# Optimization experiments

Measured on AMD Instinct MI355X. Metric: run time of the kernel, lower is better.

## Reference

```python
import jax, jax.numpy as jnp
import numpy as np

N_ING, N_DIR = 100000, 50000
E = 1000000
H, D = 4, 16          # heads, per-head dim
HID = H * D           # 64
LAT, COND = 32, 8
F_ING, F_DIR = 16, 8
OUT_ING = 16


def _han_edge(x_src, x_dst, att_s, att_d, edge_index, n_dst):
    # HANConv per-edge-type attention message passing.
    src, dst = edge_index[0], edge_index[1]
    a = jax.nn.leaky_relu(
        jnp.einsum('nhd,hd->nh', x_src, att_s)[src]
        + jnp.einsum('nhd,hd->nh', x_dst, att_d)[dst],
        negative_slope=0.2)                               # [E, H]
    amax = jax.ops.segment_max(a, dst, num_segments=n_dst)
    ex = jnp.exp(a - amax[dst])
    denom = jax.ops.segment_sum(ex, dst, num_segments=n_dst)
    alpha = ex / (denom[dst] + 1e-16)                     # PyG softmax eps
    out = jax.ops.segment_sum(x_src[src] * alpha[:, :, None], dst,
                              num_segments=n_dst)         # [n_dst, H, D]
    return jax.nn.relu(out.reshape(n_dst, HID))


def _group(outs, q, Wk, bk):
    # HANConv semantic-level attention across edge types.
    s = jnp.stack(outs)                                   # [T, N, HID]
    score = jnp.tanh(s @ Wk + bk).mean(axis=1) @ q        # [T]
    attn = jax.nn.softmax(score)
    return jnp.einsum('t,tnf->nf', attn, s)


def setup_inputs() -> dict:
    key = jax.random.key(0)
    ks = jax.random.split(key, 32)
    def ei(k, n_src, n_dst):
        k1, k2 = jax.random.split(k)
        return jnp.stack([jax.random.randint(k1, (E,), 0, n_src),
                          jax.random.randint(k2, (E,), 0, n_dst)]).astype(jnp.int64)
    s = 0.1
    inp = {
        'x_ing': jax.random.normal(ks[0], (N_ING, F_ING), jnp.float32),
        'x_dir': jax.random.normal(ks[1], (N_DIR, F_DIR), jnp.float32),
        'cond':  jax.random.normal(ks[2], (COND,), jnp.float32),
        'eps':   jax.random.normal(ks[3], (1, LAT), jnp.float32),
        'ei_cooc':     ei(ks[4], N_ING, N_DIR),
        'ei_used':     ei(ks[5], N_ING, N_DIR),
        'ei_contains': ei(ks[6], N_DIR, N_ING),
        'ei_pairs':    ei(ks[7], N_DIR, N_DIR),
        'ei_follows':  ei(ks[8], N_DIR, N_DIR),
        # node-type projections
        'W_pi': jax.random.normal(ks[9],  (F_ING, HID)) * s,
        'b_pi': jnp.zeros((HID,)),
        'W_pd': jax.random.normal(ks[10], (F_DIR, HID)) * s,
        'b_pd': jnp.zeros((HID,)),
        # semantic attention
        'Wk': jax.random.normal(ks[21], (HID, HID)) * s,
        'bk': jnp.zeros((HID,)),
        'q':  jax.random.normal(ks[22], (HID,)) * s,
        # VAE heads (input: 2*HID + COND)
        'W_mu': jax.random.normal(ks[23], (2 * HID + COND, LAT)) * s,
        'b_mu': jnp.zeros((LAT,)),
        'W_lv': jax.random.normal(ks[24], (2 * HID + COND, LAT)) * s,
        'b_lv': jnp.zeros((LAT,)),
        # decoder (fc1 is dead code in the original forward)
        'W_fc3': jax.random.normal(ks[25], (LAT, HID)) * s,
        'b_fc3': jnp.zeros((HID,)),
        'W_fc2': jax.random.normal(ks[26], (HID, OUT_ING)) * s,
        'b_fc2': jnp.zeros((OUT_ING,)),
    }
    for i, name in enumerate(['cooc', 'used', 'contains', 'pairs', 'follows']):
        inp[f'as_{name}'] = jax.random.normal(ks[11 + i], (H, D)) * s
        inp[f'ad_{name}'] = jax.random.normal(ks[16 + i], (H, D)) * s
    return inp


def reference(x_ing, x_dir, cond, eps,
              ei_cooc, ei_used, ei_contains, ei_pairs, ei_follows,
              W_pi, b_pi, W_pd, b_pd,
              as_cooc, ad_cooc, as_used, ad_used, as_contains, ad_contains,
              as_pairs, ad_pairs, as_follows, ad_follows,
              Wk, bk, q, W_mu, b_mu, W_lv, b_lv,
              W_fc3, b_fc3, W_fc2, b_fc2):
    # node-type projections -> [N, H, D]
    h_ing = (x_ing @ W_pi + b_pi).reshape(N_ING, H, D)
    h_dir = (x_dir @ W_pd + b_pd).reshape(N_DIR, H, D)

    o_cooc = _han_edge(h_ing, h_dir, as_cooc, ad_cooc, ei_cooc, N_DIR)
    o_used = _han_edge(h_ing, h_dir, as_used, ad_used, ei_used, N_DIR)
    o_cont = _han_edge(h_dir, h_ing, as_contains, ad_contains, ei_contains, N_ING)
    o_pair = _han_edge(h_dir, h_dir, as_pairs, ad_pairs, ei_pairs, N_DIR)
    o_foll = _han_edge(h_dir, h_dir, as_follows, ad_follows, ei_follows, N_DIR)

    out_ing = _group([o_cont], q, Wk, bk)                       # [N_ING, HID]
    out_dir = _group([o_cooc, o_used, o_pair, o_foll], q, Wk, bk)

    ingre_pool = out_ing.mean(axis=0, keepdims=True)            # [1, HID]
    direc_pool = out_dir.mean(axis=0, keepdims=True)
    graph_repr = jnp.concatenate([ingre_pool, direc_pool, cond[None]], axis=1)

    mu = graph_repr @ W_mu + b_mu
    logvar = graph_repr @ W_lv + b_lv
    z = mu + eps * jnp.exp(0.5 * logvar)

    # decoder: fc1 branch is overwritten in the original; effective path below
    recon = jnp.tanh(jax.nn.relu(z @ W_fc3 + b_fc3) @ W_fc2 + b_fc2)  # [1, OUT_ING]
    return recon, mu, logvar
```

## Files before the change

kernel.cpp:

```cpp
#include <hip/hip_runtime.h>
#include <hip/hip_fp16.h>
#include <math.h>

#define N_ING 100000
#define N_DIR 50000
#define NE    1000000
#define NDST_TOTAL 300000
#define NBUCK 4688
#define BA    32
#define NBK   (5 * BA)
#define I4PT  (NE / 4)
#define PB_ING 384
#define PB_DIR 192

typedef float v2f __attribute__((ext_vector_type(2)));

__global__ __launch_bounds__(256) void kA_kernel(
    const int* __restrict__ e0, const int* __restrict__ e1,
    const int* __restrict__ e2, const int* __restrict__ e3,
    const int* __restrict__ e4, int* __restrict__ blockcnt,
    const float* __restrict__ x_ing, const float* __restrict__ W_pi,
    const float* __restrict__ b_pi,
    const float* __restrict__ as_cooc, const float* __restrict__ as_used,
    const float* __restrict__ ad_contains,
    unsigned* __restrict__ h8_ing, __half* __restrict__ s_ing,
    const float* __restrict__ x_dir, const float* __restrict__ W_pd,
    const float* __restrict__ b_pd,
    const float* __restrict__ ad_cooc, const float* __restrict__ ad_used,
    const float* __restrict__ as_contains, const float* __restrict__ as_pairs,
    const float* __restrict__ ad_pairs, const float* __restrict__ as_follows,
    const float* __restrict__ ad_follows,
    unsigned* __restrict__ h8_dir, __half* __restrict__ s_dir)
{
    __shared__ int hist[NBUCK];
    __shared__ float sW[16 * 64];
    __shared__ float sbb[64];
    __shared__ float satt[7 * 64];
    __shared__ float sx[4][16];
    __shared__ float srow[4][64];

    const int bid = blockIdx.x;
    const int tid = threadIdx.x;
    if (bid < NBK) {
        const int type = bid / BA, blk = bid % BA;
        const int* ei = type == 0 ? e0 : type == 1 ? e1 : type == 2 ? e2
                      : type == 3 ? e3 : e4;
        const int base = type == 0 ? 0 : type == 1 ? 50000 : type == 2 ? 100000
                       : type == 3 ? 200000 : 250000;
        for (int i = tid; i < NBUCK; i += 256) hist[i] = 0;
        __syncthreads();
        const int4* d4 = (const int4*)(ei + NE);
        for (int i = blk * 256 + tid; i < I4PT; i += BA * 256) {
            int4 d = d4[i];
            atomicAdd(&hist[(base + d.x) >> 6], 1);
            atomicAdd(&hist[(base + d.y) >> 6], 1);
            atomicAdd(&hist[(base + d.z) >> 6], 1);
            atomicAdd(&hist[(base + d.w) >> 6], 1);
        }
        __syncthreads();
        int* row = blockcnt + (size_t)bid * NBUCK;
        for (int i = tid; i < NBUCK; i += 256) row[i] = hist[i];
    } else if (bid < NBK + PB_ING) {
        const int g = tid >> 6, t = tid & 63;
        for (int i = tid; i < 16 * 64; i += 256) sW[i] = W_pi[i];
        if (tid < 64) {
            sbb[tid] = b_pi[tid];
            satt[tid]       = as_cooc[tid];
            satt[64 + tid]  = as_used[tid];
            satt[128 + tid] = ad_contains[tid];
        }
        __syncthreads();
        for (int q = bid - NBK; q < N_ING / 4; q += PB_ING) {
            int n = q * 4 + g;
            if (t < 16) sx[g][t] = x_ing[(size_t)n * 16 + t];
            __syncthreads();
            float s = sbb[t];
#pragma unroll
            for (int i = 0; i < 16; ++i) s += sx[g][i] * sW[i * 64 + t];
            srow[g][t] = s;
            __syncthreads();
            if (t < 16) {
                int w0 = __builtin_amdgcn_cvt_pk_fp8_f32(srow[g][t * 4], srow[g][t * 4 + 1], 0, false);
                int w  = __builtin_amdgcn_cvt_pk_fp8_f32(srow[g][t * 4 + 2], srow[g][t * 4 + 3], w0, true);
                h8_ing[(size_t)n * 16 + t] = (unsigned)w;
            }
            if (t < 12) {
                int slot = t >> 2, hh = t & 3;
                float sc = 0.f;
#pragma unroll
                for (int d = 0; d < 16; ++d)
                    sc += srow[g][hh * 16 + d] * satt[slot * 64 + hh * 16 + d];
                s_ing[(size_t)n * 12 + t] = __float2half(sc);
            }
            __syncthreads();
        }
    } else {
        const int g = tid >> 6, t = tid & 63;
        for (int i = tid; i < 8 * 64; i += 256) sW[i] = W_pd[i];
        if (tid < 64) {
            sbb[tid] = b_pd[tid];
            satt[tid]        = ad_cooc[tid];
            satt[64  + tid]  = ad_used[tid];
            satt[128 + tid]  = as_contains[tid];
            satt[192 + tid]  = as_pairs[tid];
            satt[256 + tid]  = ad_pairs[tid];
            satt[320 + tid]  = as_follows[tid];
            satt[384 + tid]  = ad_follows[tid];
        }
        __syncthreads();
        for (int q = bid - NBK - PB_ING; q < N_DIR / 4; q += PB_DIR) {
            int n = q * 4 + g;
            if (t < 8) sx[g][t] = x_dir[(size_t)n * 8 + t];
            __syncthreads();
            float s = sbb[t];
#pragma unroll
            for (int i = 0; i < 8; ++i) s += sx[g][i] * sW[i * 64 + t];
            srow[g][t] = s;
            __syncthreads();
            if (t < 16) {
                int w0 = __builtin_amdgcn_cvt_pk_fp8_f32(srow[g][t * 4], srow[g][t * 4 + 1], 0, false);
                int w  = __builtin_amdgcn_cvt_pk_fp8_f32(srow[g][t * 4 + 2], srow[g][t * 4 + 3], w0, true);
                h8_dir[(size_t)n * 16 + t] = (unsigned)w;
            }
            if (t < 28) {
                int slot = t >> 2, hh = t & 3;
                float sc = 0.f;
#pragma unroll
                for (int d = 0; d < 16; ++d)
                    sc += srow[g][hh * 16 + d] * satt[slot * 64 + hh * 16 + d];
                s_dir[(size_t)n * 28 + t] = __float2half(sc);
            }
            __syncthreads();
        }
    }
}

__global__ __launch_bounds__(256) void k2_kernel(
    const int* __restrict__ blockcnt, int* __restrict__ blockbase,
    int* __restrict__ bbase, int* __restrict__ btot, int* __restrict__ cursor)
{
    __shared__ int part[4][64];
    __shared__ int tots[64];
    __shared__ int scn[64];
    __shared__ int bw;
    const int tid = threadIdx.x;
    const int kq = tid >> 6, bl = tid & 63;
    const int b = blockIdx.x * 64 + bl;
    const int K = NBK / 4;
    int ps = 0;
    if (b < NBUCK)
        for (int k = kq * K; k < kq * K + K; ++k)
            ps += blockcnt[(size_t)k * NBUCK + b];
    part[kq][bl] = ps;
    __syncthreads();
    if (tid < 64) {
        int t = part[0][tid] + part[1][tid] + part[2][tid] + part[3][tid];
        tots[tid] = t;
        scn[tid] = t;
    }
    __syncthreads();
    for (int off = 1; off < 64; off <<= 1) {
        int v = 0;
        if (tid < 64 && tid >= off) v = scn[tid - off];
        __syncthreads();
        if (tid < 64) scn[tid] += v;
        __syncthreads();
    }
    if (tid == 63) bw = atomicAdd(cursor, scn[63]);
    __syncthreads();
    if (b < NBUCK) {
        int bs = bw + scn[bl] - tots[bl];
        if (kq == 0) {
            bbase[b] = bs;
            btot[b] = tots[bl];
        }
        int run = bs;
        for (int q = 0; q < kq; ++q) run += part[q][bl];
        for (int k = kq * K; k < kq * K + K; ++k) {
            blockbase[(size_t)k * NBUCK + b] = run;
            run += blockcnt[(size_t)k * NBUCK + b];
        }
    }
}

__global__ __launch_bounds__(256) void k3_kernel(
    const int* __restrict__ e0, const int* __restrict__ e1,
    const int* __restrict__ e2, const int* __restrict__ e3,
    const int* __restrict__ e4, const int* __restrict__ blockbase,
    unsigned* __restrict__ bpair)
{
    __shared__ int cur[NBUCK];
    const int bid = blockIdx.x, tid = threadIdx.x;
    const int type = bid / BA, blk = bid % BA;
    const int* ei = type == 0 ? e0 : type == 1 ? e1 : type == 2 ? e2
                  : type == 3 ? e3 : e4;
    const int base = type == 0 ? 0 : type == 1 ? 50000 : type == 2 ? 100000
                   : type == 3 ? 200000 : 250000;
    const int* row = blockbase + (size_t)bid * NBUCK;
    for (int i = tid; i < NBUCK; i += 256) cur[i] = row[i];
    __syncthreads();
    const int4* s4 = (const int4*)ei;
    const int4* d4 = (const int4*)(ei + NE);
    for (int i = blk * 256 + tid; i < I4PT; i += BA * 256) {
        int4 s = s4[i];
        int4 d = d4[i];
        int g0 = base + d.x, g1 = base + d.y, g2 = base + d.z, g3 = base + d.w;
        int p0 = atomicAdd(&cur[g0 >> 6], 1);
        int p1 = atomicAdd(&cur[g1 >> 6], 1);
        int p2 = atomicAdd(&cur[g2 >> 6], 1);
        int p3 = atomicAdd(&cur[g3 >> 6], 1);
        bpair[p0] = ((unsigned)(g0 & 63) << 17) | (unsigned)s.x;
        bpair[p1] = ((unsigned)(g1 & 63) << 17) | (unsigned)s.y;
        bpair[p2] = ((unsigned)(g2 & 63) << 17) | (unsigned)s.z;
        bpair[p3] = ((unsigned)(g3 & 63) << 17) | (unsigned)s.w;
    }
}

__global__ __launch_bounds__(256) void k4_kernel(
    const unsigned* __restrict__ bpair, const int* __restrict__ bbase,
    const int* __restrict__ btot, int* __restrict__ perm,
    int* __restrict__ start, int* __restrict__ cnt)
{
    __shared__ int hw[4][64];
    __shared__ int sc[64];
    __shared__ int cuw[4][64];
    const int b = blockIdx.x, tid = threadIdx.x;
    const int w = tid >> 6;
    const int jb = bbase[b], n = btot[b];
    if (tid < 256) { hw[tid >> 6][tid & 63] = 0; }
    __syncthreads();
    for (int i = tid; i < n; i += 256)
        atomicAdd(&hw[w][bpair[jb + i] >> 17], 1);
    __syncthreads();
    if (tid == 0) {
        int r = 0;
        for (int i = 0; i < 64; ++i) {
            int h0 = hw[0][i], h1 = hw[1][i], h2 = hw[2][i], h3 = hw[3][i];
            sc[i] = r;
            cuw[0][i] = r;
            cuw[1][i] = r + h0;
            cuw[2][i] = r + h0 + h1;
            cuw[3][i] = r + h0 + h1 + h2;
            r += h0 + h1 + h2 + h3;
        }
    }
    __syncthreads();
    if (tid < 64) {
        int dg = b * 64 + tid;
        if (dg < NDST_TOTAL) {
            start[dg] = jb + sc[tid];
            int nx = (tid < 63) ? sc[tid + 1] : n;
            cnt[dg] = nx - sc[tid];
        }
    }
    for (int i = tid; i < n; i += 256) {
        unsigned p = bpair[jb + i];
        int pos = atomicAdd(&cuw[w][p >> 17], 1);
        perm[jb + pos] = (int)(p & 0x1FFFF);
    }
}

__global__ __launch_bounds__(256) void agg_all_kernel(
    const int* __restrict__ perm, const int* __restrict__ start,
    const int* __restrict__ cnttot,
    const unsigned* __restrict__ h8_ing, const unsigned* __restrict__ h8_dir,
    const __half* __restrict__ s_ing, const __half* __restrict__ s_dir,
    const float* __restrict__ Wk, const float* __restrict__ bk,
    float* __restrict__ pool_ing, float* __restrict__ pool_dir,
    float* __restrict__ sem_dir)
{
    __shared__ float srow[4][64];
    __shared__ float sred[4][64];
    const int t = threadIdx.x & 63, w = threadIdx.x >> 6;
    const int g  = t >> 4;
    const int l4 = t & 15;
    const int hq = l4 >> 2;
    float wkc[64];
#pragma unroll
    for (int k = 0; k < 64; ++k) wkc[k] = Wk[k * 64 + t];
    const float bkf = bk[t];
    float p_ing = 0.f;
    float p0 = 0.f, p1 = 0.f, p2 = 0.f, p3 = 0.f;
    float m0 = 0.f, m1 = 0.f, m2 = 0.f, m3 = 0.f;
    const int nwaves = gridDim.x * 4;
    for (int d = blockIdx.x * 4 + w; d < NDST_TOTAL; d += nwaves) {
        int type, ld;
        const __half *ssrc, *sdst;
        const unsigned* hsrc;
        int ss, soff, ds, doff;
        if (d < 50000)       { type = 0; ld = d;          ssrc = s_ing; ss = 12; soff = 0;  sdst = s_dir; ds = 28; doff = 0;  hsrc = h8_ing; }
        else if (d < 100000) { type = 1; ld = d - 50000;  ssrc = s_ing; ss = 12; soff = 4;  sdst = s_dir; ds = 28; doff = 4;  hsrc = h8_ing; }
        else if (d < 200000) { type = 2; ld = d - 100000; ssrc = s_dir; ss = 28; soff = 8;  sdst = s_ing; ds = 12; doff = 8;  hsrc = h8_dir; }
        else if (d < 250000) { type = 3; ld = d - 200000; ssrc = s_dir; ss = 28; soff = 12; sdst = s_dir; ds = 28; doff = 16; hsrc = h8_dir; }
        else                 { type = 4; ld = d - 250000; ssrc = s_dir; ss = 28; soff = 20; sdst = s_dir; ds = 28; doff = 24; hsrc = h8_dir; }
        float adst = __half2float(sdst[(size_t)ld * ds + doff + hq]);
        int jb = start[d], je = jb + cnttot[d];
        float4 acc = make_float4(0.f, 0.f, 0.f, 0.f);
        float dsum = 0.f;
        for (int j = jb; j < je; j += 8) {
            int j0 = j + g, j1 = j + 4 + g;
            bool v0 = j0 < je, v1 = j1 < je;
            int s0 = perm[v0 ? j0 : je - 1];
            int s1 = perm[v1 ? j1 : je - 1];
            float c0 = __half2float(ssrc[(size_t)s0 * ss + soff + hq]);
            float c1 = __half2float(ssrc[(size_t)s1 * ss + soff + hq]);
            unsigned u0 = hsrc[(size_t)s0 * 16 + l4];
            unsigned u1 = hsrc[(size_t)s1 * 16 + l4];
            float a0 = c0 + adst; a0 = a0 > 0.f ? a0 : 0.2f * a0;
            float a1 = c1 + adst; a1 = a1 > 0.f ? a1 : 0.2f * a1;
            float e0 = v0 ? __expf(a0) : 0.f;
            float e1 = v1 ? __expf(a1) : 0.f;
            dsum += e0 + e1;
            v2f lo0 = __builtin_amdgcn_cvt_pk_f32_fp8((int)u0, false);
            v2f hi0 = __builtin_amdgcn_cvt_pk_f32_fp8((int)u0, true);
            v2f lo1 = __builtin_amdgcn_cvt_pk_f32_fp8((int)u1, false);
            v2f hi1 = __builtin_amdgcn_cvt_pk_f32_fp8((int)u1, true);
            acc.x += lo0.x * e0 + lo1.x * e1;
            acc.y += lo0.y * e0 + lo1.y * e1;
            acc.z += hi0.x * e0 + hi1.x * e1;
            acc.w += hi0.y * e0 + hi1.y * e1;
        }
#pragma unroll
        for (int mask = 16; mask <= 32; mask <<= 1) {
            acc.x += __shfl_xor(acc.x, mask, 64);
            acc.y += __shfl_xor(acc.y, mask, 64);
            acc.z += __shfl_xor(acc.z, mask, 64);
            acc.w += __shfl_xor(acc.w, mask, 64);
            dsum  += __shfl_xor(dsum,  mask, 64);
        }
        float inv = 1.f / (dsum + 1e-16f);
        float4 v4 = make_float4(fmaxf(acc.x * inv, 0.f), fmaxf(acc.y * inv, 0.f),
                                fmaxf(acc.z * inv, 0.f), fmaxf(acc.w * inv, 0.f));
        if (g == 0) *(float4*)&srow[w][l4 * 4] = v4;
        float v = srow[w][t];
        if (type == 2) {
            p_ing += v;
        } else {
            float a2 = bkf;
#pragma unroll
            for (int k = 0; k < 64; ++k)
                a2 += __int_as_float(__builtin_amdgcn_readlane(__float_as_int(v), k)) * wkc[k];
            float tv = tanhf(a2);
            if (type == 0)      { p0 += v; m0 += tv; }
            else if (type == 1) { p1 += v; m1 += tv; }
            else if (type == 3) { p2 += v; m2 += tv; }
            else                { p3 += v; m3 += tv; }
        }
    }
    float vals[9] = { p_ing, p0, p1, p2, p3, m0, m1, m2, m3 };
    float* outs[9] = { pool_ing, pool_dir, pool_dir + 64, pool_dir + 128,
                       pool_dir + 192, sem_dir, sem_dir + 64, sem_dir + 128,
                       sem_dir + 192 };
    for (int i = 0; i < 9; ++i) {
        __syncthreads();
        sred[w][t] = vals[i];
        __syncthreads();
        if (w == 0)
            atomicAdd(&outs[i][t], sred[0][t] + sred[1][t] + sred[2][t] + sred[3][t]);
    }
}

__global__ __launch_bounds__(64) void final_kernel(
    const float* __restrict__ pool_ing, const float* __restrict__ pool_dir,
    const float* __restrict__ sem_dir, const float* __restrict__ q,
    const float* __restrict__ cond, const float* __restrict__ eps,
    const float* __restrict__ W_mu, const float* __restrict__ b_mu,
    const float* __restrict__ W_lv, const float* __restrict__ b_lv,
    const float* __restrict__ W_fc3, const float* __restrict__ b_fc3,
    const float* __restrict__ W_fc2, const float* __restrict__ b_fc2,
    float* __restrict__ out)
{
    __shared__ float gr[136];
    __shared__ float sc[4], attn[4];
    __shared__ float z[32], hfc[64];
    int t = threadIdx.x;
    if (t < 4) {
        float s = 0.f;
        for (int f = 0; f < 64; ++f)
            s += (sem_dir[t * 64 + f] / (float)N_DIR) * q[f];
        sc[t] = s;
    }
    gr[t] = pool_ing[t] / (float)N_ING;
    __syncthreads();
    if (t == 0) {
        float m = fmaxf(fmaxf(sc[0], sc[1]), fmaxf(sc[2], sc[3]));
        float ssum = 0.f;
        for (int i = 0; i < 4; ++i) { attn[i] = expf(sc[i] - m); ssum += attn[i]; }
        for (int i = 0; i < 4; ++i) attn[i] /= ssum;
    }
    __syncthreads();
    {
        float v = 0.f;
        for (int tt = 0; tt < 4; ++tt)
            v += attn[tt] * (pool_dir[tt * 64 + t] / (float)N_DIR);
        gr[64 + t] = v;
    }
    if (t < 8) gr[128 + t] = cond[t];
    __syncthreads();
    if (t < 32) {
        float m = b_mu[t], lv = b_lv[t];
        for (int i = 0; i < 136; ++i) {
            float g = gr[i];
            m  += g * W_mu[i * 32 + t];
            lv += g * W_lv[i * 32 + t];
        }
        out[16 + t] = m;
        out[48 + t] = lv;
        z[t] = m + eps[t] * expf(0.5f * lv);
    }
    __syncthreads();
    {
        float v = b_fc3[t];
        for (int j = 0; j < 32; ++j) v += z[j] * W_fc3[j * 64 + t];
        hfc[t] = fmaxf(v, 0.f);
    }
    __syncthreads();
    if (t < 16) {
        float v = b_fc2[t];
        for (int f = 0; f < 64; ++f) v += hfc[f] * W_fc2[f * 16 + t];
        out[t] = tanhf(v);
    }
}

extern "C" void kernel_launch(void* const* d_in, const int* in_sizes, int n_in,
                              void* d_out, int out_size, void* d_ws, size_t ws_size,
                              hipStream_t stream) {
    const float* x_ing = (const float*)d_in[0];
    const float* x_dir = (const float*)d_in[1];
    const float* cond  = (const float*)d_in[2];
    const float* eps   = (const float*)d_in[3];
    const int* ei_cooc     = (const int*)d_in[4];
    const int* ei_used     = (const int*)d_in[5];
    const int* ei_contains = (const int*)d_in[6];
    const int* ei_pairs    = (const int*)d_in[7];
    const int* ei_follows  = (const int*)d_in[8];
    const float* W_pi = (const float*)d_in[9];
    const float* b_pi = (const float*)d_in[10];
    const float* W_pd = (const float*)d_in[11];
    const float* b_pd = (const float*)d_in[12];
    const float* Wk   = (const float*)d_in[13];
    const float* bk   = (const float*)d_in[14];
    const float* q    = (const float*)d_in[15];
    const float* W_mu = (const float*)d_in[16];
    const float* b_mu = (const float*)d_in[17];
    const float* W_lv = (const float*)d_in[18];
    const float* b_lv = (const float*)d_in[19];
    const float* W_fc3 = (const float*)d_in[20];
    const float* b_fc3 = (const float*)d_in[21];
    const float* W_fc2 = (const float*)d_in[22];
    const float* b_fc2 = (const float*)d_in[23];
    const float* as_cooc     = (const float*)d_in[24];
    const float* ad_cooc     = (const float*)d_in[25];
    const float* as_used     = (const float*)d_in[26];
    const float* ad_used     = (const float*)d_in[27];
    const float* as_contains = (const float*)d_in[28];
    const float* ad_contains = (const float*)d_in[29];
    const float* as_pairs    = (const float*)d_in[30];
    const float* ad_pairs    = (const float*)d_in[31];
    const float* as_follows  = (const float*)d_in[32];
    const float* ad_follows  = (const float*)d_in[33];

    unsigned* bpair = (unsigned*)d_ws;
    unsigned* h8_ing = bpair + (size_t)5 * NE;
    unsigned* h8_dir = h8_ing + (size_t)N_ING * 16;
    __half* s_ing = (__half*)(h8_dir + (size_t)N_DIR * 16);
    __half* s_dir = s_ing + (size_t)N_ING * 12;
    int*   perm  = (int*)(s_dir + (size_t)N_DIR * 28);
    int*   blockcnt  = perm + (size_t)5 * NE;
    int*   blockbase = blockcnt + (size_t)NBK * NBUCK;
    int*   bbase  = blockbase + (size_t)NBK * NBUCK;
    int*   btot   = bbase + NBUCK;
    int*   start  = btot + NBUCK;
    int*   cnt    = start + NDST_TOTAL;
    int*   cursor = cnt + NDST_TOTAL;
    float* pool_ing = (float*)(cursor + 1);
    float* pool_dir = pool_ing + 64;
    float* sem_dir  = pool_dir + 256;

    hipMemsetAsync(cursor, 0, (1 + 64 + 256 + 256) * sizeof(int), stream);

    kA_kernel<<<NBK + PB_ING + PB_DIR, 256, 0, stream>>>(
        ei_cooc, ei_used, ei_contains, ei_pairs, ei_follows, blockcnt,
        x_ing, W_pi, b_pi, as_cooc, as_used, ad_contains, h8_ing, s_ing,
        x_dir, W_pd, b_pd, ad_cooc, ad_used, as_contains, as_pairs, ad_pairs,
        as_follows, ad_follows, h8_dir, s_dir);

    k2_kernel<<<(NBUCK + 63) / 64, 256, 0, stream>>>(
        blockcnt, blockbase, bbase, btot, cursor);

    k3_kernel<<<NBK, 256, 0, stream>>>(
        ei_cooc, ei_used, ei_contains, ei_pairs, ei_follows, blockbase, bpair);

    k4_kernel<<<NBUCK, 256, 0, stream>>>(bpair, bbase, btot, perm, start, cnt);

    agg_all_kernel<<<2048, 256, 0, stream>>>(
        perm, start, cnt, h8_ing, h8_dir, s_ing, s_dir, Wk, bk,
        pool_ing, pool_dir, sem_dir);

    final_kernel<<<1, 64, 0, stream>>>(
        pool_ing, pool_dir, sem_dir, q, cond, eps,
        W_mu, b_mu, W_lv, b_lv, W_fc3, b_fc3, W_fc2, b_fc2, (float*)d_out);
}
```

Before: 591.8 us.

## Batch semantic-attention matvecs four rows at a time with Wk in LDS

Wk is staged in shared memory instead of 64 per-thread registers. The 64x64 tanh projection is batched over four destination rows per wave, so each Wk load is reused across four rows. Each wave now handles a contiguous range of destinations instead of a strided one, so it can collect the non-ingredient rows into batches. The bucket count constant BA is halved, which changes the bucketing granularity of the sort phase. This lowers register pressure and readlane work, which may raise occupancy, at the cost of LDS traffic and more LDS use per block.

New measurement: 1.217 ms. 106% more time.

```diff
diff --git a/kernel.cpp b/kernel.cpp
--- a/kernel.cpp
+++ b/kernel.cpp
@@ -7,7 +7,7 @@
 #define NE    1000000
 #define NDST_TOTAL 300000
 #define NBUCK 4688
-#define BA    32
+#define BA    16
 #define NBK   (5 * BA)
 #define I4PT  (NE / 4)
 #define PB_ING 384
@@ -227,7 +227,7 @@
     const int b = blockIdx.x, tid = threadIdx.x;
     const int w = tid >> 6;
     const int jb = bbase[b], n = btot[b];
-    if (tid < 256) { hw[tid >> 6][tid & 63] = 0; }
+    hw[tid >> 6][tid & 63] = 0;
     __syncthreads();
     for (int i = tid; i < n; i += 256)
         atomicAdd(&hw[w][bpair[jb + i] >> 17], 1);
@@ -269,21 +269,30 @@
     float* __restrict__ pool_ing, float* __restrict__ pool_dir,
     float* __restrict__ sem_dir)
 {
-    __shared__ float srow[4][64];
+    __shared__ float sWk[64 * 64];
+    __shared__ float srow4[4][4][64];
     __shared__ float sred[4][64];
     const int t = threadIdx.x & 63, w = threadIdx.x >> 6;
     const int g  = t >> 4;
     const int l4 = t & 15;
     const int hq = l4 >> 2;
-    float wkc[64];
-#pragma unroll
-    for (int k = 0; k < 64; ++k) wkc[k] = Wk[k * 64 + t];
+    for (int i = threadIdx.x; i < 4096; i += 256) sWk[i] = Wk[i];
     const float bkf = bk[t];
     float p_ing = 0.f;
     float p0 = 0.f, p1 = 0.f, p2 = 0.f, p3 = 0.f;
     float m0 = 0.f, m1 = 0.f, m2 = 0.f, m3 = 0.f;
+    __syncthreads();
+
     const int nwaves = gridDim.x * 4;
-    for (int d = blockIdx.x * 4 + w; d < NDST_TOTAL; d += nwaves) {
+    const int wave_id = blockIdx.x * 4 + w;
+    const int spw = (NDST_TOTAL + nwaves - 1) / nwaves;
+    const int dlo = wave_id * spw;
+    const int dhi = min(dlo + spw, NDST_TOTAL);
+
+    int nb = 0;
+    int btype[4];
+
+    for (int d = dlo; d < dhi; ++d) {
         int type, ld;
         const __half *ssrc, *sdst;
         const unsigned* hsrc;
@@ -331,22 +340,76 @@
         float inv = 1.f / (dsum + 1e-16f);
         float4 v4 = make_float4(fmaxf(acc.x * inv, 0.f), fmaxf(acc.y * inv, 0.f),
                                 fmaxf(acc.z * inv, 0.f), fmaxf(acc.w * inv, 0.f));
-        if (g == 0) *(float4*)&srow[w][l4 * 4] = v4;
-        float v = srow[w][t];
+        if (g == 0) *(float4*)&srow4[w][nb][l4 * 4] = v4;
         if (type == 2) {
-            p_ing += v;
+            p_ing += srow4[w][nb][t];
         } else {
-            float a2 = bkf;
-#pragma unroll
-            for (int k = 0; k < 64; ++k)
-                a2 += __int_as_float(__builtin_amdgcn_readlane(__float_as_int(v), k)) * wkc[k];
-            float tv = tanhf(a2);
-            if (type == 0)      { p0 += v; m0 += tv; }
-            else if (type == 1) { p1 += v; m1 += tv; }
-            else if (type == 3) { p2 += v; m2 += tv; }
-            else                { p3 += v; m3 += tv; }
-        }
-    }
+            btype[nb] = type;
+            ++nb;
+            if (nb == 4) {
+                float a20 = bkf, a21 = bkf, a22 = bkf, a23 = bkf;
+#pragma unroll
+                for (int kc = 0; kc < 16; ++kc) {
+                    float w0 = sWk[(kc * 4 + 0) * 64 + t];
+                    float w1 = sWk[(kc * 4 + 1) * 64 + t];
+                    float w2 = sWk[(kc * 4 + 2) * 64 + t];
+                    float w3 = sWk[(kc * 4 + 3) * 64 + t];
+                    float4 r0 = *(float4*)&srow4[w][0][kc * 4];
+                    float4 r1 = *(float4*)&srow4[w][1][kc * 4];
+                    float4 r2 = *(float4*)&srow4[w][2][kc * 4];
+                    float4 r3 = *(float4*)&srow4[w][3][kc * 4];
+                    a20 += r0.x * w0 + r0.y * w1 + r0.z * w2 + r0.w * w3;
+                    a21 += r1.x * w0 + r1.y * w1 + r1.z * w2 + r1.w * w3;
+                    a22 += r2.x * w0 + r2.y * w1 + r2.z * w2 + r2.w * w3;
+                    a23 += r3.x * w0 + r3.y * w1 + r3.z * w2 + r3.w * w3;
+                }
+                float a2v[4] = { a20, a21, a22, a23 };
+#pragma unroll
+                for (int r = 0; r < 4; ++r) {
+                    float tv = tanhf(a2v[r]);
+                    float vr = srow4[w][r][t];
+                    int ty = btype[r];
+                    if (ty == 0)      { p0 += vr; m0 += tv; }
+                    else if (ty == 1) { p1 += vr; m1 += tv; }
+                    else if (ty == 3) { p2 += vr; m2 += tv; }
+                    else              { p3 += vr; m3 += tv; }
+                }
+                nb = 0;
+            }
+        }
+    }
+    if (nb > 0) {
+        float a20 = bkf, a21 = bkf, a22 = bkf, a23 = bkf;
+#pragma unroll
+        for (int kc = 0; kc < 16; ++kc) {
+            float w0 = sWk[(kc * 4 + 0) * 64 + t];
+            float w1 = sWk[(kc * 4 + 1) * 64 + t];
+            float w2 = sWk[(kc * 4 + 2) * 64 + t];
+            float w3 = sWk[(kc * 4 + 3) * 64 + t];
+            float4 r0 = *(float4*)&srow4[w][0][kc * 4];
+            float4 r1 = *(float4*)&srow4[w][1][kc * 4];
+            float4 r2 = *(float4*)&srow4[w][2][kc * 4];
+            float4 r3 = *(float4*)&srow4[w][3][kc * 4];
+            a20 += r0.x * w0 + r0.y * w1 + r0.z * w2 + r0.w * w3;
+            a21 += r1.x * w0 + r1.y * w1 + r1.z * w2 + r1.w * w3;
+            a22 += r2.x * w0 + r2.y * w1 + r2.z * w2 + r2.w * w3;
+            a23 += r3.x * w0 + r3.y * w1 + r3.z * w2 + r3.w * w3;
+        }
+        float a2v[4] = { a20, a21, a22, a23 };
+#pragma unroll
+        for (int r = 0; r < 4; ++r) {
+            if (r < nb) {
+                float tv = tanhf(a2v[r]);
+                float vr = srow4[w][r][t];
+                int ty = btype[r];
+                if (ty == 0)      { p0 += vr; m0 += tv; }
+                else if (ty == 1) { p1 += vr; m1 += tv; }
+                else if (ty == 3) { p2 += vr; m2 += tv; }
+                else              { p3 += vr; m3 += tv; }
+            }
+        }
+    }
+
     float vals[9] = { p_ing, p0, p1, p2, p3, m0, m1, m2, m3 };
     float* outs[9] = { pool_ing, pool_dir, pool_dir + 64, pool_dir + 128,
                        pool_dir + 192, sem_dir, sem_dir + 64, sem_dir + 128,
```

## Specialize aggregation per edge type via templates and stage Wk in LDS

Applied to the files above, without the earlier changes.

Splits the per-destination loop of the aggregation kernel into five templated range loops, one per edge type, so strides and offsets become compile-time constants and the per-iteration type branching disappears. The 64-register per-thread copy of Wk is replaced by a shared-memory copy read during the semantic projection, which frees many registers and should raise occupancy, at the cost of LDS reads in place of readlane broadcasts. The bucket-count constant BA is halved, changing the granularity of the bucketing stage. Index arithmetic switches to 32-bit unsigned.

Measured after the change: 606.1 us. 1.02x slower.

```diff
diff --git a/kernel.cpp b/kernel.cpp
--- a/kernel.cpp
+++ b/kernel.cpp
@@ -7,7 +7,7 @@
 #define NE    1000000
 #define NDST_TOTAL 300000
 #define NBUCK 4688
-#define BA    32
+#define BA    16
 #define NBK   (5 * BA)
 #define I4PT  (NE / 4)
 #define PB_ING 384
@@ -227,7 +227,7 @@
     const int b = blockIdx.x, tid = threadIdx.x;
     const int w = tid >> 6;
     const int jb = bbase[b], n = btot[b];
-    if (tid < 256) { hw[tid >> 6][tid & 63] = 0; }
+    hw[tid >> 6][tid & 63] = 0;
     __syncthreads();
     for (int i = tid; i < n; i += 256)
         atomicAdd(&hw[w][bpair[jb + i] >> 17], 1);
@@ -260,52 +260,32 @@
     }
 }
 
-__global__ __launch_bounds__(256) void agg_all_kernel(
+template<int SS, int SOFF, int DS, int DOFF, bool SEM>
+__device__ __forceinline__ void agg_range(
+    int dlo, int dhi, int wave, int nwaves,
+    int t, int w, int g, int l4, int hq,
     const int* __restrict__ perm, const int* __restrict__ start,
-    const int* __restrict__ cnttot,
-    const unsigned* __restrict__ h8_ing, const unsigned* __restrict__ h8_dir,
-    const __half* __restrict__ s_ing, const __half* __restrict__ s_dir,
-    const float* __restrict__ Wk, const float* __restrict__ bk,
-    float* __restrict__ pool_ing, float* __restrict__ pool_dir,
-    float* __restrict__ sem_dir)
-{
-    __shared__ float srow[4][64];
-    __shared__ float sred[4][64];
-    const int t = threadIdx.x & 63, w = threadIdx.x >> 6;
-    const int g  = t >> 4;
-    const int l4 = t & 15;
-    const int hq = l4 >> 2;
-    float wkc[64];
-#pragma unroll
-    for (int k = 0; k < 64; ++k) wkc[k] = Wk[k * 64 + t];
-    const float bkf = bk[t];
-    float p_ing = 0.f;
-    float p0 = 0.f, p1 = 0.f, p2 = 0.f, p3 = 0.f;
-    float m0 = 0.f, m1 = 0.f, m2 = 0.f, m3 = 0.f;
-    const int nwaves = gridDim.x * 4;
-    for (int d = blockIdx.x * 4 + w; d < NDST_TOTAL; d += nwaves) {
-        int type, ld;
-        const __half *ssrc, *sdst;
-        const unsigned* hsrc;
-        int ss, soff, ds, doff;
-        if (d < 50000)       { type = 0; ld = d;          ssrc = s_ing; ss = 12; soff = 0;  sdst = s_dir; ds = 28; doff = 0;  hsrc = h8_ing; }
-        else if (d < 100000) { type = 1; ld = d - 50000;  ssrc = s_ing; ss = 12; soff = 4;  sdst = s_dir; ds = 28; doff = 4;  hsrc = h8_ing; }
-        else if (d < 200000) { type = 2; ld = d - 100000; ssrc = s_dir; ss = 28; soff = 8;  sdst = s_ing; ds = 12; doff = 8;  hsrc = h8_dir; }
-        else if (d < 250000) { type = 3; ld = d - 200000; ssrc = s_dir; ss = 28; soff = 12; sdst = s_dir; ds = 28; doff = 16; hsrc = h8_dir; }
-        else                 { type = 4; ld = d - 250000; ssrc = s_dir; ss = 28; soff = 20; sdst = s_dir; ds = 28; doff = 24; hsrc = h8_dir; }
-        float adst = __half2float(sdst[(size_t)ld * ds + doff + hq]);
-        int jb = start[d], je = jb + cnttot[d];
+    const int* __restrict__ cnt,
+    const unsigned* __restrict__ hsrc, const __half* __restrict__ ssrc,
+    const __half* __restrict__ sdst,
+    const float* sWk, float bkf, float (*srow)[64],
+    float& pool, float& sem)
+{
+    for (int d = dlo + wave; d < dhi; d += nwaves) {
+        unsigned ld = (unsigned)(d - dlo);
+        float adst = __half2float(sdst[ld * DS + DOFF + hq]);
+        int jb = start[d], je = jb + cnt[d];
         float4 acc = make_float4(0.f, 0.f, 0.f, 0.f);
         float dsum = 0.f;
         for (int j = jb; j < je; j += 8) {
             int j0 = j + g, j1 = j + 4 + g;
             bool v0 = j0 < je, v1 = j1 < je;
-            int s0 = perm[v0 ? j0 : je - 1];
-            int s1 = perm[v1 ? j1 : je - 1];
-            float c0 = __half2float(ssrc[(size_t)s0 * ss + soff + hq]);
-            float c1 = __half2float(ssrc[(size_t)s1 * ss + soff + hq]);
-            unsigned u0 = hsrc[(size_t)s0 * 16 + l4];
-            unsigned u1 = hsrc[(size_t)s1 * 16 + l4];
+            unsigned s0 = (unsigned)perm[v0 ? j0 : je - 1];
+            unsigned s1 = (unsigned)perm[v1 ? j1 : je - 1];
+            float c0 = __half2float(ssrc[s0 * SS + (SOFF + hq)]);
+            float c1 = __half2float(ssrc[s1 * SS + (SOFF + hq)]);
+            unsigned u0 = hsrc[s0 * 16 + l4];
+            unsigned u1 = hsrc[s1 * 16 + l4];
             float a0 = c0 + adst; a0 = a0 > 0.f ? a0 : 0.2f * a0;
             float a1 = c1 + adst; a1 = a1 > 0.f ? a1 : 0.2f * a1;
             float e0 = v0 ? __expf(a0) : 0.f;
@@ -333,20 +313,51 @@
                                 fmaxf(acc.z * inv, 0.f), fmaxf(acc.w * inv, 0.f));
         if (g == 0) *(float4*)&srow[w][l4 * 4] = v4;
         float v = srow[w][t];
-        if (type == 2) {
-            p_ing += v;
-        } else {
+        pool += v;
+        if (SEM) {
             float a2 = bkf;
 #pragma unroll
-            for (int k = 0; k < 64; ++k)
-                a2 += __int_as_float(__builtin_amdgcn_readlane(__float_as_int(v), k)) * wkc[k];
-            float tv = tanhf(a2);
-            if (type == 0)      { p0 += v; m0 += tv; }
-            else if (type == 1) { p1 += v; m1 += tv; }
-            else if (type == 3) { p2 += v; m2 += tv; }
-            else                { p3 += v; m3 += tv; }
-        }
-    }
+            for (int k = 0; k < 64; ++k) a2 += srow[w][k] * sWk[k * 64 + t];
+            sem += tanhf(a2);
+        }
+    }
+}
+
+__global__ __launch_bounds__(256) void agg_all_kernel(
+    const int* __restrict__ perm, const int* __restrict__ start,
+    const int* __restrict__ cnt,
+    const unsigned* __restrict__ h8_ing, const unsigned* __restrict__ h8_dir,
+    const __half* __restrict__ s_ing, const __half* __restrict__ s_dir,
+    const float* __restrict__ Wk, const float* __restrict__ bk,
+    float* __restrict__ pool_ing, float* __restrict__ pool_dir,
+    float* __restrict__ sem_dir)
+{
+    __shared__ float sWk[64 * 64];
+    __shared__ float srow[4][64];
+    __shared__ float sred[4][64];
+    const int t = threadIdx.x & 63, w = threadIdx.x >> 6;
+    const int g  = t >> 4;
+    const int l4 = t & 15;
+    const int hq = l4 >> 2;
+    for (int i = threadIdx.x; i < 4096; i += 256) sWk[i] = Wk[i];
+    const float bkf = bk[t];
+    float p_ing = 0.f, dummy = 0.f;
+    float p0 = 0.f, p1 = 0.f, p2 = 0.f, p3 = 0.f;
+    float m0 = 0.f, m1 = 0.f, m2 = 0.f, m3 = 0.f;
+    __syncthreads();
+    const int nwaves = gridDim.x * 4;
+    const int wave = blockIdx.x * 4 + w;
+    agg_range<12, 0, 28, 0,  true>(0,      50000,  wave, nwaves, t, w, g, l4, hq,
+        perm, start, cnt, h8_ing, s_ing, s_dir, sWk, bkf, srow, p0, m0);
+    agg_range<12, 4, 28, 4,  true>(50000,  100000, wave, nwaves, t, w, g, l4, hq,
+        perm, start, cnt, h8_ing, s_ing, s_dir, sWk, bkf, srow, p1, m1);
+    agg_range<28, 8, 12, 8,  false>(100000, 200000, wave, nwaves, t, w, g, l4, hq,
+        perm, start, cnt, h8_dir, s_dir, s_ing, sWk, bkf, srow, p_ing, dummy);
+    agg_range<28, 12, 28, 16, true>(200000, 250000, wave, nwaves, t, w, g, l4, hq,
+        perm, start, cnt, h8_dir, s_dir, s_dir, sWk, bkf, srow, p2, m2);
+    agg_range<28, 20, 28, 24, true>(250000, 300000, wave, nwaves, t, w, g, l4, hq,
+        perm, start, cnt, h8_dir, s_dir, s_dir, sWk, bkf, srow, p3, m3);
+
     float vals[9] = { p_ing, p0, p1, p2, p3, m0, m1, m2, m3 };
     float* outs[9] = { pool_ing, pool_dir, pool_dir + 64, pool_dir + 128,
                        pool_dir + 192, sem_dir, sem_dir + 64, sem_dir + 128,
```
